# Kernel optimization log

Measured on AMD Instinct MI355X. Metric: run time of the kernel, lower is better.

Reference implementation:

```python
import jax, jax.numpy as jnp
import numpy as np


def setup_inputs() -> dict:
    key = jax.random.key(0)
    k1, k2, k3 = jax.random.split(key, 3)
    RAW_NODES = 40962          # ico-6 sphere
    NUM_NODES = RAW_NODES * 4 - 6   # 163842, ico-7 sphere
    FEAT = 256
    x = jax.random.normal(k1, (RAW_NODES, FEAT), dtype=jnp.float32)
    max_index = jax.random.randint(k2, (RAW_NODES, FEAT), 0, 7, dtype=jnp.int64)
    neigh_orders = jax.random.randint(k3, (RAW_NODES * 7,), 0, NUM_NODES, dtype=jnp.int64)
    return {"x": x, "max_index": max_index, "neigh_orders": neigh_orders, "num_nodes": NUM_NODES}


def reference(x, max_index, neigh_orders, num_nodes):
    raw_nodes, feat_num = x.shape
    # column_ref[i, f] = i*7 + max_index[i, f]  (vectorized form of the python loop)
    column_ref = (jnp.arange(raw_nodes, dtype=max_index.dtype)[:, None] * 7 + max_index).reshape(-1)
    column_index = neigh_orders[column_ref]  # gather from neighborhood lookup table
    # row_index exactly as in the original: floor(linspace(0, feat_num, raw_nodes*feat_num)), last clamped
    row_index = np.floor(np.linspace(0.0, float(feat_num), num=raw_nodes * feat_num)).astype(np.int64)
    row_index[-1] = row_index[-1] - 1
    row_index = jnp.asarray(row_index)
    y = jnp.zeros((num_nodes, feat_num), dtype=x.dtype)
    # scatter: y[column_index, row_index] = x.view(-1)
    y = y.at[column_index, row_index].set(x.reshape(-1))
    return y
```

## Files before the change

### kernel.cpp

```cpp
#include <hip/hip_runtime.h>
#include <stdint.h>


#define FEAT 256
#define LOG2FEAT 8
#define BLOCK 256
#define ROW_WGS 256
#define HASH 2048
#define LOG2HASH 11

typedef float f32x4 __attribute__((ext_vector_type(4)));

extern "C" __global__ __launch_bounds__(BLOCK)
void zero_counts_kernel(int* __restrict__ count, int n)
{
    for (int idx = blockIdx.x * BLOCK + threadIdx.x; idx < n;
         idx += gridDim.x * BLOCK)
        count[idx] = 0;
}

extern "C" __global__ __launch_bounds__(BLOCK)
void row_build_kernel(const int*   __restrict__ mi,
                      const int*   __restrict__ neigh,
                      const float* __restrict__ x,
                      int2*        __restrict__ table,
                      int*         __restrict__ count,
                      int total,
                      int cap)
{
    __shared__ int hkey[HASH];
    __shared__ int hval[HASH];

    const int tid = threadIdx.x;
    for (int s = tid; s < HASH; s += BLOCK) { hkey[s] = -1; hval[s] = 0; }
    __syncthreads();

    const int r = blockIdx.x;
    const unsigned tm1 = (unsigned)(total - 1);
    const unsigned klo = ((unsigned)r * tm1 + 255u) >> 8;
    const unsigned khi = (r == 255) ? (unsigned)(total - 1)
                       : (((unsigned)(r + 1) * tm1 + 255u) >> 8) - 1u;
    const int i0 = (int)(klo >> 8);
    const int i1 = (int)(khi >> 8);

    const int lane = tid & 63;
    const int wv   = tid >> 6;

    int p0 = 0, p1 = 0, p2 = 0, p3 = 0;
    {
        const int ifirst = i0 + wv;
        if (ifirst <= i1) {
            const int* mrow = mi + (ifirst << LOG2FEAT);
            p0 = mrow[lane];       p1 = mrow[64 + lane];
            p2 = mrow[128 + lane]; p3 = mrow[192 + lane];
        }
    }

    for (int i = i0 + wv; i <= i1; i += 4) {
        const int m0 = p0, m1 = p1, m2 = p2, m3 = p3;
        const int inx = i + 4;
        if (inx <= i1) {
            const int* mrow = mi + (inx << LOG2FEAT);
            p0 = mrow[lane];       p1 = mrow[64 + lane];
            p2 = mrow[128 + lane]; p3 = mrow[192 + lane];
        }
        const int mycol = (lane < 7) ? neigh[i * 7 + lane] : 0;

        const int kbase = i << LOG2FEAT;
        int wlo = (int)klo - kbase; if (wlo < 0)   wlo = 0;
        int whi = (int)khi - kbase; if (whi > 255) whi = 255;

        unsigned long long wm[4];
        #pragma unroll
        for (int j = 0; j < 4; ++j) {
            int lo = wlo - j * 64;  if (lo < 0) lo = 0;
            int hi = whi - j * 64 + 1;
            unsigned long long mhi = (hi >= 64) ? ~0ull
                                   : (hi <= 0)  ? 0ull : ((1ull << hi) - 1ull);
            unsigned long long mlo = (lo >= 64) ? ~0ull : ((1ull << lo) - 1ull);
            wm[j] = mhi & ~mlo;
        }

        unsigned long long b[4][7];
        #pragma unroll
        for (int m = 0; m < 7; ++m) {
            b[0][m] = __ballot(m0 == m);
            b[1][m] = __ballot(m1 == m);
            b[2][m] = __ballot(m2 == m);
            b[3][m] = __ballot(m3 == m);
        }

        if (lane < 7) {
            const int m = lane;
            int bestf = -1;
            #pragma unroll
            for (int j = 3; j >= 0; --j) {
                if (bestf < 0) {
                    unsigned long long s =
                        (m == 0) ? b[j][0] : (m == 1) ? b[j][1] :
                        (m == 2) ? b[j][2] : (m == 3) ? b[j][3] :
                        (m == 4) ? b[j][4] : (m == 5) ? b[j][5] : b[j][6];
                    unsigned long long t = s & wm[j];
                    if (t) bestf = j * 64 + 63 - __clzll(t);
                }
            }
            if (bestf >= 0) {
                const int kp1 = kbase + bestf + 1;
                int slot = mycol & (HASH - 1);
                while (true) {
                    int prev = atomicCAS(&hkey[slot], -1, mycol);
                    if (prev == -1 || prev == mycol) {
                        atomicMax(&hval[slot], kp1);
                        break;
                    }
                    slot = (slot + 1) & (HASH - 1);
                }
            }
        }
    }

    __syncthreads();

    for (int s = tid; s < HASH; s += BLOCK) {
        const int key = hkey[s];
        if (key >= 0) {
            const int kp1  = hval[s];
            const int bits = __float_as_int(x[kp1 - 1]);
            const int slot = atomicAdd(&count[key], 1);
            if (slot < cap)
                table[(size_t)key * cap + slot] = make_int2(r, bits);
        }
    }
}

extern "C" __global__ __launch_bounds__(BLOCK)
void compose_kernel(float*      __restrict__ out,
                    const int2* __restrict__ table,
                    const int*  __restrict__ count,
                    int nnodes, int cap)
{
    const int lane   = threadIdx.x & 63;
    const int wv     = (blockIdx.x * BLOCK + threadIdx.x) >> 6;
    const int nwaves = gridDim.x * (BLOCK / 64);

    for (int n = wv; n < nnodes; n += nwaves) {
        int c = count[n];
        if (c > cap) c = cap;
        int2 e = make_int2(-1, 0);
        if (lane < c) e = table[(size_t)n * cap + lane];

        int f0 = 0, f1 = 0, f2 = 0, f3 = 0;
        for (int j = 0; j < c; ++j) {
            const int rj = __shfl(e.x, j);
            const int bj = __shfl(e.y, j);
            if ((rj >> 2) == lane) {
                const int q = rj & 3;
                if      (q == 0) f0 = bj;
                else if (q == 1) f1 = bj;
                else if (q == 2) f2 = bj;
                else             f3 = bj;
            }
        }
        f32x4 f;
        f.x = __int_as_float(f0); f.y = __int_as_float(f1);
        f.z = __int_as_float(f2); f.w = __int_as_float(f3);
        f32x4* dst = (f32x4*)(out + ((size_t)n << LOG2FEAT)) + lane;
        __builtin_nontemporal_store(f, dst);
    }
}

extern "C" void kernel_launch(void* const* d_in, const int* in_sizes, int n_in,
                              void* d_out, int out_size, void* d_ws, size_t ws_size,
                              hipStream_t stream) {
    const float* x     = (const float*)d_in[0];
    const int*   mi    = (const int*)d_in[1];
    const int*   neigh = (const int*)d_in[2];
    float*       out   = (float*)d_out;

    const int total  = in_sizes[0];
    const int nnodes = out_size >> LOG2FEAT;

    int cap = 32;
    while (cap > 8 &&
           (size_t)nnodes * (size_t)cap * sizeof(int2) + (size_t)nnodes * 4
               > ws_size)
        cap >>= 1;

    int2* table = (int2*)d_ws;
    int*  count = (int*)((char*)d_ws +
                         (size_t)nnodes * (size_t)cap * sizeof(int2));

    zero_counts_kernel<<<dim3(512), dim3(BLOCK), 0, stream>>>(count, nnodes);
    row_build_kernel<<<dim3(ROW_WGS), dim3(BLOCK), 0, stream>>>(
        mi, neigh, x, table, count, total, cap);
    compose_kernel<<<dim3(2048), dim3(BLOCK), 0, stream>>>(
        out, table, count, nnodes, cap);
}
```

Baseline: 306.8 us.

## Split each row's scan across several workgroups and resolve last writer in compose

```diff
diff --git a/kernel.cpp b/kernel.cpp
--- a/kernel.cpp
+++ b/kernel.cpp
@@ -5,10 +5,9 @@
 #define FEAT 256
 #define LOG2FEAT 8
 #define BLOCK 256
-#define ROW_WGS 256
-#define HASH 2048
-#define LOG2HASH 11
-
+#define NROWS 256
+#define SPLIT 8
+#define HASH 512
 typedef float f32x4 __attribute__((ext_vector_type(4)));
 
 extern "C" __global__ __launch_bounds__(BLOCK)
@@ -35,31 +34,36 @@
     for (int s = tid; s < HASH; s += BLOCK) { hkey[s] = -1; hval[s] = 0; }
     __syncthreads();
 
-    const int r = blockIdx.x;
+    const int r   = blockIdx.x / SPLIT;
+    const int sub = blockIdx.x % SPLIT;
     const unsigned tm1 = (unsigned)(total - 1);
     const unsigned klo = ((unsigned)r * tm1 + 255u) >> 8;
     const unsigned khi = (r == 255) ? (unsigned)(total - 1)
                        : (((unsigned)(r + 1) * tm1 + 255u) >> 8) - 1u;
     const int i0 = (int)(klo >> 8);
     const int i1 = (int)(khi >> 8);
+    const int len   = i1 - i0 + 1;
+    const int chunk = (len + SPLIT - 1) / SPLIT;
+    const int ia = i0 + sub * chunk;
+    int ib = ia + chunk - 1; if (ib > i1) ib = i1;
 
     const int lane = tid & 63;
     const int wv   = tid >> 6;
 
     int p0 = 0, p1 = 0, p2 = 0, p3 = 0;
     {
-        const int ifirst = i0 + wv;
-        if (ifirst <= i1) {
+        const int ifirst = ia + wv;
+        if (ifirst <= ib) {
             const int* mrow = mi + (ifirst << LOG2FEAT);
             p0 = mrow[lane];       p1 = mrow[64 + lane];
             p2 = mrow[128 + lane]; p3 = mrow[192 + lane];
         }
     }
 
-    for (int i = i0 + wv; i <= i1; i += 4) {
+    for (int i = ia + wv; i <= ib; i += 4) {
         const int m0 = p0, m1 = p1, m2 = p2, m3 = p3;
         const int inx = i + 4;
-        if (inx <= i1) {
+        if (inx <= ib) {
             const int* mrow = mi + (inx << LOG2FEAT);
             p0 = mrow[lane];       p1 = mrow[64 + lane];
             p2 = mrow[128 + lane]; p3 = mrow[192 + lane];
@@ -128,7 +132,8 @@
             const int bits = __float_as_int(x[kp1 - 1]);
             const int slot = atomicAdd(&count[key], 1);
             if (slot < cap)
-                table[(size_t)key * cap + slot] = make_int2(r, bits);
+                table[(size_t)key * cap + slot] =
+                    make_int2((int)(((unsigned)kp1 << 8) | (unsigned)r), bits);
         }
     }
 }
@@ -146,26 +151,28 @@
     for (int n = wv; n < nnodes; n += nwaves) {
         int c = count[n];
         if (c > cap) c = cap;
-        int2 e = make_int2(-1, 0);
+        int2 e = make_int2(0, 0);
         if (lane < c) e = table[(size_t)n * cap + lane];
 
+        unsigned k0 = 0, k1 = 0, k2 = 0, k3 = 0;
         int f0 = 0, f1 = 0, f2 = 0, f3 = 0;
         for (int j = 0; j < c; ++j) {
-            const int rj = __shfl(e.x, j);
-            const int bj = __shfl(e.y, j);
+            const unsigned ex = (unsigned)__shfl(e.x, j);
+            const int      bj = __shfl(e.y, j);
+            const int      rj = (int)(ex & 255u);
             if ((rj >> 2) == lane) {
                 const int q = rj & 3;
-                if      (q == 0) f0 = bj;
-                else if (q == 1) f1 = bj;
-                else if (q == 2) f2 = bj;
-                else             f3 = bj;
+                if      (q == 0) { if (ex > k0) { k0 = ex; f0 = bj; } }
+                else if (q == 1) { if (ex > k1) { k1 = ex; f1 = bj; } }
+                else if (q == 2) { if (ex > k2) { k2 = ex; f2 = bj; } }
+                else             { if (ex > k3) { k3 = ex; f3 = bj; } }
             }
         }
         f32x4 f;
         f.x = __int_as_float(f0); f.y = __int_as_float(f1);
         f.z = __int_as_float(f2); f.w = __int_as_float(f3);
         f32x4* dst = (f32x4*)(out + ((size_t)n << LOG2FEAT)) + lane;
-        __builtin_nontemporal_store(f, dst);
+        *dst = f;
     }
 }
 
@@ -190,8 +197,8 @@
     int*  count = (int*)((char*)d_ws +
                          (size_t)nnodes * (size_t)cap * sizeof(int2));
 
-    zero_counts_kernel<<<dim3(512), dim3(BLOCK), 0, stream>>>(count, nnodes);
-    row_build_kernel<<<dim3(ROW_WGS), dim3(BLOCK), 0, stream>>>(
+    zero_counts_kernel<<<dim3(256), dim3(BLOCK), 0, stream>>>(count, nnodes);
+    row_build_kernel<<<dim3(NROWS * SPLIT), dim3(BLOCK), 0, stream>>>(
         mi, neigh, x, table, count, total, cap);
     compose_kernel<<<dim3(2048), dim3(BLOCK), 0, stream>>>(
         out, table, count, nnodes, cap);
```

Result: faster. 281.3 us (-8.3%).
